# Kernel tuning notes

Hardware: AMD Instinct MI355X
Metric: run time of the kernel (lower is better)

The kernel has to match this reference:

```python
import jax, jax.numpy as jnp
import numpy as np

T = 1024
B = 64
A = 128
ABSTRACT_PENALTY = 0.5
CONSISTENCY_RATIO = 1.0
NEG = -1e30  # acts as log(0) mask; exp underflows to exactly 0 in logsumexp
STOP_IX, CONT_IX = 0, 1


def setup_inputs() -> dict:
    key = jax.random.key(0)
    k1, k2, k3, k4, k5 = jax.random.split(key, 5)
    actions = jax.random.randint(k1, (T,), 0, A, dtype=jnp.int32)
    action_logps = jax.nn.log_softmax(jax.random.normal(k2, (T + 1, B, A), dtype=jnp.float32), axis=-1)
    stop_logps = jax.nn.log_softmax(jax.random.normal(k3, (T + 1, B, 2), dtype=jnp.float32), axis=-1)
    start_logps = jax.nn.log_softmax(jax.random.normal(k4, (T + 1, B), dtype=jnp.float32), axis=-1)
    consistency_penalties = -0.1 * jnp.abs(jax.random.normal(k5, (T + 1, T + 1, B), dtype=jnp.float32))
    return {
        'actions': actions,
        'action_logps': action_logps,
        'stop_logps': stop_logps,
        'start_logps': start_logps,
        'consistency_penalties': consistency_penalties,
    }


def _hsmm_loss(actions, action_logps, stop_logps, start_logps, consistency_penalties):
    T_ = actions.shape[0]
    b = start_logps.shape[1]
    # option_step_dist as fixed (T, b) buffer, rows > current step masked to NEG
    dist0 = jnp.full((T_, b), NEG, dtype=action_logps.dtype).at[0].set(start_logps[0])
    # step i=0: only the action logp (no stop/start rearrange, no consistency pen)
    logp0 = jax.nn.logsumexp(dist0 + action_logps[0, :, actions[0]][None, :])

    idx = jnp.arange(1, T_)
    stop_lps = stop_logps[1:T_, :, STOP_IX]          # (T-1, b)
    cont_lps = stop_logps[1:T_, :, CONT_IX]          # (T-1, b)
    start_lps = start_logps[1:T_]                    # (T-1, b)
    act_lps = action_logps[idx, :, actions[1:]]      # (T-1, b)
    # column i of consistency_penalties, rows :T (masked dist rows kill rows > i)
    cons_cols = jnp.transpose(consistency_penalties[:T_, 1:T_, :], (1, 0, 2))  # (T-1, T, b)

    def step(carry, xs):
        dist, logp, cons = carry
        i, stop_lp, cont_lp, start_lp, act_lp, cp = xs
        total_rearrange = jax.nn.logsumexp(dist + stop_lp[None, :]) - ABSTRACT_PENALTY
        new_mass = start_lp + total_rearrange
        dist = (dist + cont_lp[None, :]).at[i].set(new_mass)
        cons = cons + jax.nn.logsumexp(dist + cp)
        logp = logp + jax.nn.logsumexp(dist + act_lp[None, :])
        return (dist, logp, cons), None

    init = (dist0, logp0, jnp.zeros((), dist0.dtype))
    (dist, logp, cons), _ = jax.lax.scan(step, init, (idx, stop_lps, cont_lps, start_lps, act_lps, cons_cols))
    total_logp = logp + jax.nn.logsumexp(dist + stop_logps[T_, :, STOP_IX][None, :])
    return -total_logp + CONSISTENCY_RATIO * cons


def reference(actions, action_logps, stop_logps, start_logps, consistency_penalties):
    return _hsmm_loss(actions, action_logps, stop_logps, start_logps, consistency_penalties)
```

## Files before the change

kernel.cpp:

```cpp
#include <hip/hip_runtime.h>

#define T_N 1024
#define B_N 64
#define A_N 128
#define TP1 1025

typedef float f32x4 __attribute__((ext_vector_type(4)));

__device__ __forceinline__ float bcf(int x){ return __builtin_bit_cast(float, x); }
__device__ __forceinline__ int   bci(float x){ return __builtin_bit_cast(int, x); }

template<int CTRL, int RM>
__device__ __forceinline__ float dpp_add_step(float x){
  int t = __builtin_amdgcn_update_dpp(0, bci(x), CTRL, RM, 0xf, true);
  return x + bcf(t);
}
__device__ __forceinline__ float wave_sum64(float x){
  x = dpp_add_step<0x111,0xf>(x);
  x = dpp_add_step<0x112,0xf>(x);
  x = dpp_add_step<0x114,0xf>(x);
  x = dpp_add_step<0x118,0xf>(x);
  x = dpp_add_step<0x142,0xa>(x);
  x = dpp_add_step<0x143,0xc>(x);
  return bcf(__builtin_amdgcn_readlane(bci(x), 63));
}
__device__ __forceinline__ void wave_sum64_x2(float a, float b, float& ra, float& rb){
  a = dpp_add_step<0x111,0xf>(a);  b = dpp_add_step<0x111,0xf>(b);
  a = dpp_add_step<0x112,0xf>(a);  b = dpp_add_step<0x112,0xf>(b);
  a = dpp_add_step<0x114,0xf>(a);  b = dpp_add_step<0x114,0xf>(b);
  a = dpp_add_step<0x118,0xf>(a);  b = dpp_add_step<0x118,0xf>(b);
  a = dpp_add_step<0x142,0xa>(a);  b = dpp_add_step<0x142,0xa>(b);
  a = dpp_add_step<0x143,0xc>(a);  b = dpp_add_step<0x143,0xc>(b);
  ra = bcf(__builtin_amdgcn_readlane(bci(a), 63));
  rb = bcf(__builtin_amdgcn_readlane(bci(b), 63));
}
__device__ __forceinline__ float group16_sum(float x){
  x = dpp_add_step<0x111,0xf>(x);
  x = dpp_add_step<0x112,0xf>(x);
  x = dpp_add_step<0x114,0xf>(x);
  x = dpp_add_step<0x118,0xf>(x);
  return x;
}
template<int CTRL, int RM>
__device__ __forceinline__ float dpp_max_step(float x){
  int t = __builtin_amdgcn_update_dpp(bci(-3.4e38f), bci(x), CTRL, RM, 0xf, false);
  return fmaxf(x, bcf(t));
}
__device__ __forceinline__ float wave_max64(float x){
  x = dpp_max_step<0x111,0xf>(x);
  x = dpp_max_step<0x112,0xf>(x);
  x = dpp_max_step<0x114,0xf>(x);
  x = dpp_max_step<0x118,0xf>(x);
  x = dpp_max_step<0x142,0xa>(x);
  x = dpp_max_step<0x143,0xc>(x);
  return bcf(__builtin_amdgcn_readlane(bci(x), 63));
}

__global__ __launch_bounds__(256) void prep_kernel(
    const float* __restrict__ stop_logps,
    const float* __restrict__ start_logps,
    float* __restrict__ pairA,
    float* __restrict__ kap,
    float* __restrict__ cs,
    float* __restrict__ A1p)
{
  const int tid  = (int)threadIdx.x;
  const int lane = tid & 63;
  const int wv   = tid >> 6;
  const int p    = (int)blockIdx.x * 4 + wv;
  const float KAPPA = 0.60653065971263342f;
  const float2* stop2 = (const float2*)stop_logps;

  int g = (int)blockIdx.x * 256 + tid;
  A1p[g] = 0.f;
  A1p[g + 32768] = 0.f;

  if (p < 511) {
    const int i1 = 2 * p + 1, i2 = 2 * p + 2;
    float2 s1 = stop2[i1 * B_N + lane];
    float2 s2 = stop2[i2 * B_N + lane];
    float st1 = start_logps[i1 * B_N + lane];
    float st2 = start_logps[i2 * B_N + lane];
    float esw1 = __expf(s1.x), ecw1 = __expf(s1.y), sv1 = KAPPA * __expf(st1);
    float esw2 = __expf(s2.x), ecw2 = __expf(s2.y), sv2 = KAPPA * __expf(st2);
    float* pb = pairA + (size_t)p * 7 * B_N;
    pb[0 * B_N + lane] = esw1;
    pb[1 * B_N + lane] = ecw1 * esw2;
    pb[2 * B_N + lane] = ecw1 * ecw2;
    pb[3 * B_N + lane] = sv1 * ecw2;
    pb[4 * B_N + lane] = sv1;
    pb[5 * B_N + lane] = sv2;
    pb[6 * B_N + lane] = ecw1;
    float kp = wave_sum64(sv1 * esw2);
    if (lane == 0) kap[p] = kp;
  }

  if (blockIdx.x < 16 && wv == 0) {
    int c = (int)blockIdx.x;
    float s = 0.f;
    for (int k = 1; k <= 64; ++k) {
      int i = 64 * c + k;
      if (i <= 1023) s += stop2[i * B_N + lane].y;
    }
    cs[c * B_N + lane] = s;
  }
}

__global__ __launch_bounds__(64, 1) void scan_kernel(
    const float* __restrict__ stop_logps,
    const float* __restrict__ start_logps,
    const float* __restrict__ pairA,
    const float* __restrict__ kap,
    float* __restrict__ z_ws,
    float* __restrict__ r_ws,
    float* __restrict__ wexp)
{
  const int lane = threadIdx.x;
  float z = __expf(start_logps[lane]);

  float pb[8][7];
  float kp[8];
  #pragma unroll
  for (int q = 0; q < 8; ++q) {
    #pragma unroll
    for (int v = 0; v < 7; ++v) pb[q][v] = pairA[(q * 7 + v) * B_N + lane];
    kp[q] = kap[q];
  }

  for (int P0 = 0; P0 < 504; P0 += 8) {
    #pragma unroll
    for (int q = 0; q < 8; ++q) {
      const int p  = P0 + q;
      const int i1 = 2 * p + 1;
      float A  = pb[q][0], Q  = pb[q][1], CC = pb[q][2], SC = pb[q][3];
      float SV1= pb[q][4], SV2= pb[q][5], E1 = pb[q][6];
      float kpp = kp[q];
      #pragma unroll
      for (int v = 0; v < 7; ++v) pb[q][v] = pairA[((size_t)(p + 8) * 7 + v) * B_N + lane];
      kp[q] = kap[p + 8 < 512 ? p + 8 : 511];

      float d1, d2;
      wave_sum64_x2(z * A, z * Q, d1, d2);
      float r2 = __builtin_fmaf(kpp, d1, d2);
      float z1 = __builtin_fmaf(d1, SV1, z * E1);
      z_ws[i1 * B_N + lane] = z1;
      r_ws[i1]     = d1;
      r_ws[i1 + 1] = r2;
      z = __builtin_fmaf(z, CC, __builtin_fmaf(r2, SV2, d1 * SC));
      z_ws[(i1 + 1) * B_N + lane] = z;

      if (q == 7) {
        int rb  = bci(r2);
        int e16 = ((rb >> 23) & 255) - 127;
        z = ldexpf(z, -e16);
        wexp[p >> 3] = (float)e16;
      }
    }
  }
  #pragma unroll
  for (int q = 0; q < 7; ++q) {
    const int p  = 504 + q;
    const int i1 = 2 * p + 1;
    float A  = pb[q][0], Q  = pb[q][1], CC = pb[q][2], SC = pb[q][3];
    float SV1= pb[q][4], SV2= pb[q][5], E1 = pb[q][6];
    float kpp = kp[q];
    float d1, d2;
    wave_sum64_x2(z * A, z * Q, d1, d2);
    float r2 = __builtin_fmaf(kpp, d1, d2);
    float z1 = __builtin_fmaf(d1, SV1, z * E1);
    z_ws[i1 * B_N + lane] = z1;
    r_ws[i1]     = d1;
    r_ws[i1 + 1] = r2;
    z = __builtin_fmaf(z, CC, __builtin_fmaf(r2, SV2, d1 * SC));
    z_ws[(i1 + 1) * B_N + lane] = z;
  }
  {
    const float KAPPA = 0.60653065971263342f;
    const float2* stop2 = (const float2*)stop_logps;
    float2 sc = stop2[1023 * B_N + lane];
    float  st = start_logps[1023 * B_N + lane];
    float esw = __expf(sc.x), ecw = __expf(sc.y), sv = KAPPA * __expf(st);
    float r = wave_sum64(z * esw);
    z = __builtin_fmaf(sv, r, z * ecw);
    z_ws[1023 * B_N + lane] = z;
    r_ws[1023] = r;
  }
}

__global__ __launch_bounds__(1024) void post_kernel(
    const int* __restrict__ actions,
    const float* __restrict__ action_logps,
    const float* __restrict__ stop_logps,
    const float* __restrict__ start_logps,
    const float* __restrict__ z_ws,
    const float* __restrict__ r_ws,
    const float* __restrict__ wexp,
    const float* __restrict__ cs,
    float* __restrict__ u_ws,
    float* __restrict__ D_ws,
    float* __restrict__ out)
{
  const int tid  = (int)threadIdx.x;
  const int w    = tid >> 6;
  const int lane = tid & 63;
  const float LN2 = 0.69314718055994531f;
  const float2* stop2 = (const float2*)stop_logps;

  __shared__ float Pw[64];
  if (w == 0) {
    float psum = 0.f;
    for (int m = 0; m < lane && m < 63; ++m) psum += wexp[m];
    Pw[lane] = psum * LN2;
  }
  __syncthreads();

  float C = 0.f;
  for (int ww = 0; ww < w; ++ww) C += cs[ww * B_N + lane];
  for (int k = 1; k <= 64; ++k) {
    int i = 64 * w + k;
    if (i > 1023) break;
    C += stop2[i * B_N + lane].y;
    float Pv = Pw[(i - 1) >> 4];
    float R  = __logf(r_ws[i]) + Pv - 0.5f;
    u_ws[i * B_N + lane] = start_logps[i * B_N + lane] + R - C;
    float zs = wave_sum64(z_ws[i * B_N + lane]);
    D_ws[i * B_N + lane] = C - (__logf(zs) + Pv);
  }
  if (tid < 64) u_ws[lane] = start_logps[lane];

  if (w == 15) {
    float st0 = start_logps[lane];
    int   a0  = actions[0];
    float al0 = action_logps[lane * A_N + a0];
    float lp0 = __logf(wave_sum64(__expf(st0 + al0)));
    float stopT = stop_logps[(T_N * B_N + lane) * 2 + 0];
    float z1023 = z_ws[1023 * B_N + lane];
    float fin = __logf(wave_sum64(z1023 * __expf(stopT))) + Pw[63];
    if (lane == 0) out[0] = -(lp0 + fin);
  }
}

__global__ __launch_bounds__(256) void cons_logp_kernel(
    const float* __restrict__ cons_pen,
    const float* __restrict__ u_ws,
    const float* __restrict__ D_ws,
    const int* __restrict__ actions,
    const float* __restrict__ action_logps,
    float* __restrict__ A1p,
    float* __restrict__ LQ)
{
  const int bid  = (int)blockIdx.x;
  const int tid  = (int)threadIdx.x;
  const int lane = tid & 63;
  const int wv   = tid >> 6;

  __shared__ float sm[4][64];
  __shared__ float sa[4][64];

  if (bid < 512) {
    const int bq  = (lane & 15) * 4;
    const int row = lane >> 4;
    #pragma unroll
    for (int t = 0; t < 2; ++t) {
      const int j = t ? (1023 - bid) : bid;
      const float4 u4 = *(const float4*)(u_ws + j * B_N + bq);
      float* dst = A1p + ((j & 63) << 10);
      for (int i0 = j + 4 * wv; i0 <= 1023; i0 += 16) {
        int i  = i0 + row;
        int iL = i > 1023 ? 1023 : i;
        f32x4 cp4 = __builtin_nontemporal_load(
            (const f32x4*)(cons_pen + ((size_t)j * TP1 + iL) * B_N + bq));
        float4 d4  = *(const float4*)(D_ws + (size_t)iL * B_N + bq);
        bool valid = (i >= 1) && (i <= 1023);
        float a0 = u4.x + d4.x + cp4.x;
        float a1 = u4.y + d4.y + cp4.y;
        float a2 = u4.z + d4.z + cp4.z;
        float a3 = u4.w + d4.w + cp4.w;
        a0 = valid ? a0 : -1e30f;
        a1 = valid ? a1 : -1e30f;
        a2 = valid ? a2 : -1e30f;
        a3 = valid ? a3 : -1e30f;
        float sred = (__expf(a0) + __expf(a1)) + (__expf(a2) + __expf(a3));
        sred = group16_sum(sred);
        if (((lane & 15) == 15) && valid) atomicAdd(dst + i, sred);
      }
    }
  } else {
    const int i = 1535 - bid;
    int   ai = actions[i];
    float av = action_logps[((size_t)i * B_N + lane) * A_N + ai];

    float m = -1e30f, acc = 0.f;
    for (int jj = wv; jj <= i; jj += 4) {
      float u  = u_ws[jj * B_N + lane];
      float nm = fmaxf(m, u);
      acc = acc * __expf(m - nm) + __expf(u - nm);
      m = nm;
    }
    sm[wv][lane] = m; sa[wv][lane] = acc;
    __syncthreads();
    if (wv == 0) {
      float m0 = sm[0][lane], m1 = sm[1][lane], m2 = sm[2][lane], m3 = sm[3][lane];
      float M2 = fmaxf(fmaxf(m0, m1), fmaxf(m2, m3));
      float A  = sa[0][lane] * __expf(m0 - M2) + sa[1][lane] * __expf(m1 - M2)
               + sa[2][lane] * __expf(m2 - M2) + sa[3][lane] * __expf(m3 - M2);
      float S  = M2 + __logf(A);
      float val = S + D_ws[(size_t)i * B_N + lane] + av;
      float mx  = wave_max64(val);
      float sum = wave_sum64(__expf(val - mx));
      if (lane == 0) LQ[i] = mx + __logf(sum);
    }
  }
}

__global__ __launch_bounds__(256) void finish_kernel(
    const float* __restrict__ A1p,
    const float* __restrict__ LQ,
    float* __restrict__ out)
{
  const int i = (int)blockIdx.x * 256 + (int)threadIdx.x;
  float v = 0.f;
  if (i >= 1 && i <= 1023) {
    float a = 0.f;
    #pragma unroll 8
    for (int p = 0; p < 64; ++p) a += A1p[(p << 10) + i];
    v = __logf(a) - LQ[i];
  }
  float ws = wave_sum64(v);
  __shared__ float sb[4];
  if ((threadIdx.x & 63) == 0) sb[threadIdx.x >> 6] = ws;
  __syncthreads();
  if (threadIdx.x == 0) atomicAdd(out, sb[0] + sb[1] + sb[2] + sb[3]);
}

extern "C" void kernel_launch(void* const* d_in, const int* in_sizes, int n_in,
                              void* d_out, int out_size, void* d_ws, size_t ws_size,
                              hipStream_t stream) {
  const int*   actions      = (const int*)d_in[0];
  const float* action_logps = (const float*)d_in[1];
  const float* stop_logps   = (const float*)d_in[2];
  const float* start_logps  = (const float*)d_in[3];
  const float* cons_pen     = (const float*)d_in[4];
  float* out = (float*)d_out;

  float* z_ws  = (float*)d_ws;
  float* u_ws  = z_ws + T_N * B_N;
  float* D_ws  = u_ws + T_N * B_N;
  float* A1p   = D_ws + T_N * B_N;
  float* r_ws  = A1p + 64 * 1024;
  float* wexp  = r_ws + T_N;
  float* LQ    = wexp + 64;
  float* cs    = LQ + T_N;
  float* pairA = cs + 16 * B_N;
  float* kap   = pairA + 512 * 7 * B_N;

  hipLaunchKernelGGL(prep_kernel, dim3(128), dim3(256), 0, stream,
                     stop_logps, start_logps, pairA, kap, cs, A1p);
  hipLaunchKernelGGL(scan_kernel, dim3(1), dim3(64), 0, stream,
                     stop_logps, start_logps, pairA, kap, z_ws, r_ws, wexp);
  hipLaunchKernelGGL(post_kernel, dim3(1), dim3(1024), 0, stream,
                     actions, action_logps, stop_logps, start_logps,
                     z_ws, r_ws, wexp, cs, u_ws, D_ws, out);
  hipLaunchKernelGGL(cons_logp_kernel, dim3(1535), dim3(256), 0, stream,
                     cons_pen, u_ws, D_ws, actions, action_logps, A1p, LQ);
  hipLaunchKernelGGL(finish_kernel, dim3(4), dim3(256), 0, stream,
                     A1p, LQ, out);
}
```

Measured before the change: 524.2 us.

## Block the sequential scan four steps at a time with precomputed coupling coefficients

The single-wave sequential scan now advances four time steps per iteration instead of two. Prep precomputes the per-quad products and the cross-step coupling sums, so each iteration needs only one interleaved four-way wave reduction. This shortens the serial dependency chain of DPP reductions on the critical path, at the cost of more prep work and more registers. The r_ws indexing shifts by one and is matched in post_kernel, and the logp accumulation loop in cons_logp_kernel is split into two independent online-logsumexp chains to expose more ILP.

```diff
diff --git a/kernel.cpp b/kernel.cpp
--- a/kernel.cpp
+++ b/kernel.cpp
@@ -24,15 +24,24 @@
   x = dpp_add_step<0x143,0xc>(x);
   return bcf(__builtin_amdgcn_readlane(bci(x), 63));
 }
-__device__ __forceinline__ void wave_sum64_x2(float a, float b, float& ra, float& rb){
-  a = dpp_add_step<0x111,0xf>(a);  b = dpp_add_step<0x111,0xf>(b);
-  a = dpp_add_step<0x112,0xf>(a);  b = dpp_add_step<0x112,0xf>(b);
-  a = dpp_add_step<0x114,0xf>(a);  b = dpp_add_step<0x114,0xf>(b);
-  a = dpp_add_step<0x118,0xf>(a);  b = dpp_add_step<0x118,0xf>(b);
-  a = dpp_add_step<0x142,0xa>(a);  b = dpp_add_step<0x142,0xa>(b);
-  a = dpp_add_step<0x143,0xc>(a);  b = dpp_add_step<0x143,0xc>(b);
+__device__ __forceinline__ void wave_sum64_x4(float a, float b, float c, float d,
+                                              float& ra, float& rb, float& rc, float& rd){
+  a = dpp_add_step<0x111,0xf>(a); b = dpp_add_step<0x111,0xf>(b);
+  c = dpp_add_step<0x111,0xf>(c); d = dpp_add_step<0x111,0xf>(d);
+  a = dpp_add_step<0x112,0xf>(a); b = dpp_add_step<0x112,0xf>(b);
+  c = dpp_add_step<0x112,0xf>(c); d = dpp_add_step<0x112,0xf>(d);
+  a = dpp_add_step<0x114,0xf>(a); b = dpp_add_step<0x114,0xf>(b);
+  c = dpp_add_step<0x114,0xf>(c); d = dpp_add_step<0x114,0xf>(d);
+  a = dpp_add_step<0x118,0xf>(a); b = dpp_add_step<0x118,0xf>(b);
+  c = dpp_add_step<0x118,0xf>(c); d = dpp_add_step<0x118,0xf>(d);
+  a = dpp_add_step<0x142,0xa>(a); b = dpp_add_step<0x142,0xa>(b);
+  c = dpp_add_step<0x142,0xa>(c); d = dpp_add_step<0x142,0xa>(d);
+  a = dpp_add_step<0x143,0xc>(a); b = dpp_add_step<0x143,0xc>(b);
+  c = dpp_add_step<0x143,0xc>(c); d = dpp_add_step<0x143,0xc>(d);
   ra = bcf(__builtin_amdgcn_readlane(bci(a), 63));
   rb = bcf(__builtin_amdgcn_readlane(bci(b), 63));
+  rc = bcf(__builtin_amdgcn_readlane(bci(c), 63));
+  rd = bcf(__builtin_amdgcn_readlane(bci(d), 63));
 }
 __device__ __forceinline__ float group16_sum(float x){
   x = dpp_add_step<0x111,0xf>(x);
@@ -59,8 +68,7 @@
 __global__ __launch_bounds__(256) void prep_kernel(
     const float* __restrict__ stop_logps,
     const float* __restrict__ start_logps,
-    float* __restrict__ pairA,
-    float* __restrict__ kap,
+    float* __restrict__ quadQ,
     float* __restrict__ cs,
     float* __restrict__ A1p)
 {
@@ -72,27 +80,42 @@
   const float2* stop2 = (const float2*)stop_logps;
 
   int g = (int)blockIdx.x * 256 + tid;
-  A1p[g] = 0.f;
-  A1p[g + 32768] = 0.f;
-
-  if (p < 511) {
-    const int i1 = 2 * p + 1, i2 = 2 * p + 2;
-    float2 s1 = stop2[i1 * B_N + lane];
-    float2 s2 = stop2[i2 * B_N + lane];
-    float st1 = start_logps[i1 * B_N + lane];
-    float st2 = start_logps[i2 * B_N + lane];
-    float esw1 = __expf(s1.x), ecw1 = __expf(s1.y), sv1 = KAPPA * __expf(st1);
-    float esw2 = __expf(s2.x), ecw2 = __expf(s2.y), sv2 = KAPPA * __expf(st2);
-    float* pb = pairA + (size_t)p * 7 * B_N;
-    pb[0 * B_N + lane] = esw1;
-    pb[1 * B_N + lane] = ecw1 * esw2;
-    pb[2 * B_N + lane] = ecw1 * ecw2;
-    pb[3 * B_N + lane] = sv1 * ecw2;
-    pb[4 * B_N + lane] = sv1;
-    pb[5 * B_N + lane] = sv2;
-    pb[6 * B_N + lane] = ecw1;
-    float kp = wave_sum64(sv1 * esw2);
-    if (lane == 0) kap[p] = kp;
+  A1p[g] = 0.f; A1p[g + 16384] = 0.f; A1p[g + 32768] = 0.f; A1p[g + 49152] = 0.f;
+
+  if (p < 255) {
+    const int i1 = 4 * p + 1;
+    float2 q1 = stop2[(i1 + 0) * B_N + lane];
+    float2 q2 = stop2[(i1 + 1) * B_N + lane];
+    float2 q3 = stop2[(i1 + 2) * B_N + lane];
+    float2 q4 = stop2[(i1 + 3) * B_N + lane];
+    float t1 = start_logps[(i1 + 0) * B_N + lane];
+    float t2 = start_logps[(i1 + 1) * B_N + lane];
+    float t3 = start_logps[(i1 + 2) * B_N + lane];
+    float t4 = start_logps[(i1 + 3) * B_N + lane];
+    float e1 = __expf(q1.x), c1 = __expf(q1.y), s1 = KAPPA * __expf(t1);
+    float e2 = __expf(q2.x), c2 = __expf(q2.y), s2 = KAPPA * __expf(t2);
+    float e3 = __expf(q3.x), c3 = __expf(q3.y), s3 = KAPPA * __expf(t3);
+    float e4 = __expf(q4.x), c4 = __expf(q4.y), s4 = KAPPA * __expf(t4);
+
+    float V1 = e1;
+    float V2 = e2 * c1;
+    float V3 = e3 * c2 * c1;
+    float V4 = e4 * c3 * c2 * c1;
+
+    float k21 = wave_sum64(e2 * s1);
+    float k31 = wave_sum64(e3 * c2 * s1);
+    float k32 = wave_sum64(e3 * s2);
+    float k41 = wave_sum64(e4 * c3 * c2 * s1);
+    float k42 = wave_sum64(e4 * c3 * s2);
+    float k43 = wave_sum64(e4 * s3);
+
+    f32x4* qs = (f32x4*)quadQ;
+    size_t base = (size_t)p * 5 * 64 + lane;
+    qs[base + 0 * 64] = (f32x4){V1, V2, V3, V4};
+    qs[base + 1 * 64] = (f32x4){c1, s1, c2, s2};
+    qs[base + 2 * 64] = (f32x4){c3, s3, c4, s4};
+    qs[base + 3 * 64] = (f32x4){k21, k31, k32, k41};
+    qs[base + 4 * 64] = (f32x4){k42, k43, 0.f, 0.f};
   }
 
   if (blockIdx.x < 16 && wv == 0) {
@@ -109,81 +132,130 @@
 __global__ __launch_bounds__(64, 1) void scan_kernel(
     const float* __restrict__ stop_logps,
     const float* __restrict__ start_logps,
-    const float* __restrict__ pairA,
-    const float* __restrict__ kap,
+    const float* __restrict__ quadQ,
     float* __restrict__ z_ws,
     float* __restrict__ r_ws,
     float* __restrict__ wexp)
 {
   const int lane = threadIdx.x;
+  const float2* stop2 = (const float2*)stop_logps;
+
+  float2 sct0 = stop2[1021 * B_N + lane];
+  float2 sct1 = stop2[1022 * B_N + lane];
+  float2 sct2 = stop2[1023 * B_N + lane];
+  float stt0 = start_logps[1021 * B_N + lane];
+  float stt1 = start_logps[1022 * B_N + lane];
+  float stt2 = start_logps[1023 * B_N + lane];
+
   float z = __expf(start_logps[lane]);
 
-  float pb[8][7];
-  float kp[8];
+  const f32x4* qs = (const f32x4*)quadQ;
+
+  f32x4 qb[8][5];
   #pragma unroll
-  for (int q = 0; q < 8; ++q) {
+  for (int q = 0; q < 8; ++q)
     #pragma unroll
-    for (int v = 0; v < 7; ++v) pb[q][v] = pairA[(q * 7 + v) * B_N + lane];
-    kp[q] = kap[q];
-  }
-
-  for (int P0 = 0; P0 < 504; P0 += 8) {
+    for (int s = 0; s < 5; ++s)
+      qb[q][s] = qs[((size_t)q * 5 + s) * 64 + lane];
+
+  for (int p0 = 0; p0 < 248; p0 += 8) {
     #pragma unroll
     for (int q = 0; q < 8; ++q) {
-      const int p  = P0 + q;
-      const int i1 = 2 * p + 1;
-      float A  = pb[q][0], Q  = pb[q][1], CC = pb[q][2], SC = pb[q][3];
-      float SV1= pb[q][4], SV2= pb[q][5], E1 = pb[q][6];
-      float kpp = kp[q];
-      #pragma unroll
-      for (int v = 0; v < 7; ++v) pb[q][v] = pairA[((size_t)(p + 8) * 7 + v) * B_N + lane];
-      kp[q] = kap[p + 8 < 512 ? p + 8 : 511];
-
-      float d1, d2;
-      wave_sum64_x2(z * A, z * Q, d1, d2);
-      float r2 = __builtin_fmaf(kpp, d1, d2);
-      float z1 = __builtin_fmaf(d1, SV1, z * E1);
-      z_ws[i1 * B_N + lane] = z1;
-      r_ws[i1]     = d1;
-      r_ws[i1 + 1] = r2;
-      z = __builtin_fmaf(z, CC, __builtin_fmaf(r2, SV2, d1 * SC));
-      z_ws[(i1 + 1) * B_N + lane] = z;
-
-      if (q == 7) {
-        int rb  = bci(r2);
+      const int p  = p0 + q;
+      const int i1 = 4 * p + 1;
+      f32x4 V   = qb[q][0];
+      f32x4 C12 = qb[q][1];
+      f32x4 C34 = qb[q][2];
+      f32x4 K1  = qb[q][3];
+      f32x4 K2  = qb[q][4];
+      {
+        const int pn = p + 8;
+        #pragma unroll
+        for (int s = 0; s < 5; ++s)
+          qb[q][s] = qs[((size_t)pn * 5 + s) * 64 + lane];
+      }
+
+      float d1, d2, d3, d4;
+      wave_sum64_x4(z * V.x, z * V.y, z * V.z, z * V.w, d1, d2, d3, d4);
+      float r1 = d1;
+      float r2 = __builtin_fmaf(K1.x, r1, d2);
+      float r3 = __builtin_fmaf(K1.z, r2, __builtin_fmaf(K1.y, r1, d3));
+      float r4 = __builtin_fmaf(K2.y, r3,
+                 __builtin_fmaf(K2.x, r2, __builtin_fmaf(K1.w, r1, d4)));
+
+      float z1 = __builtin_fmaf(r1, C12.y, z  * C12.x);
+      float z2 = __builtin_fmaf(r2, C12.w, z1 * C12.z);
+      float z3 = __builtin_fmaf(r3, C34.y, z2 * C34.x);
+      float z4 = __builtin_fmaf(r4, C34.w, z3 * C34.z);
+      z_ws[(i1 + 0) * B_N + lane] = z1;
+      z_ws[(i1 + 1) * B_N + lane] = z2;
+      z_ws[(i1 + 2) * B_N + lane] = z3;
+      z_ws[(i1 + 3) * B_N + lane] = z4;
+      if (lane == 0) *(f32x4*)(r_ws + 4 * p) = (f32x4){r1, r2, r3, r4};
+      z = z4;
+
+      if ((q & 3) == 3) {
+        int rb  = bci(r4);
         int e16 = ((rb >> 23) & 255) - 127;
         z = ldexpf(z, -e16);
-        wexp[p >> 3] = (float)e16;
+        if (lane == 0) wexp[p >> 2] = (float)e16;
       }
     }
   }
   #pragma unroll
   for (int q = 0; q < 7; ++q) {
-    const int p  = 504 + q;
-    const int i1 = 2 * p + 1;
-    float A  = pb[q][0], Q  = pb[q][1], CC = pb[q][2], SC = pb[q][3];
-    float SV1= pb[q][4], SV2= pb[q][5], E1 = pb[q][6];
-    float kpp = kp[q];
-    float d1, d2;
-    wave_sum64_x2(z * A, z * Q, d1, d2);
-    float r2 = __builtin_fmaf(kpp, d1, d2);
-    float z1 = __builtin_fmaf(d1, SV1, z * E1);
-    z_ws[i1 * B_N + lane] = z1;
-    r_ws[i1]     = d1;
-    r_ws[i1 + 1] = r2;
-    z = __builtin_fmaf(z, CC, __builtin_fmaf(r2, SV2, d1 * SC));
-    z_ws[(i1 + 1) * B_N + lane] = z;
-  }
+    const int p  = 248 + q;
+    const int i1 = 4 * p + 1;
+    f32x4 V   = qb[q][0];
+    f32x4 C12 = qb[q][1];
+    f32x4 C34 = qb[q][2];
+    f32x4 K1  = qb[q][3];
+    f32x4 K2  = qb[q][4];
+    float d1, d2, d3, d4;
+    wave_sum64_x4(z * V.x, z * V.y, z * V.z, z * V.w, d1, d2, d3, d4);
+    float r1 = d1;
+    float r2 = __builtin_fmaf(K1.x, r1, d2);
+    float r3 = __builtin_fmaf(K1.z, r2, __builtin_fmaf(K1.y, r1, d3));
+    float r4 = __builtin_fmaf(K2.y, r3,
+               __builtin_fmaf(K2.x, r2, __builtin_fmaf(K1.w, r1, d4)));
+    float z1 = __builtin_fmaf(r1, C12.y, z  * C12.x);
+    float z2 = __builtin_fmaf(r2, C12.w, z1 * C12.z);
+    float z3 = __builtin_fmaf(r3, C34.y, z2 * C34.x);
+    float z4 = __builtin_fmaf(r4, C34.w, z3 * C34.z);
+    z_ws[(i1 + 0) * B_N + lane] = z1;
+    z_ws[(i1 + 1) * B_N + lane] = z2;
+    z_ws[(i1 + 2) * B_N + lane] = z3;
+    z_ws[(i1 + 3) * B_N + lane] = z4;
+    if (lane == 0) *(f32x4*)(r_ws + 4 * p) = (f32x4){r1, r2, r3, r4};
+    z = z4;
+    if (q == 3) {
+      int rb  = bci(r4);
+      int e16 = ((rb >> 23) & 255) - 127;
+      z = ldexpf(z, -e16);
+      if (lane == 0) wexp[62] = (float)e16;
+    }
+  }
+  const float KAPPA = 0.60653065971263342f;
   {
-    const float KAPPA = 0.60653065971263342f;
-    const float2* stop2 = (const float2*)stop_logps;
-    float2 sc = stop2[1023 * B_N + lane];
-    float  st = start_logps[1023 * B_N + lane];
-    float esw = __expf(sc.x), ecw = __expf(sc.y), sv = KAPPA * __expf(st);
+    float esw = __expf(sct0.x), ecw = __expf(sct0.y), sv = KAPPA * __expf(stt0);
+    float r = wave_sum64(z * esw);
+    z = __builtin_fmaf(sv, r, z * ecw);
+    z_ws[1021 * B_N + lane] = z;
+    if (lane == 0) r_ws[1020] = r;
+  }
+  {
+    float esw = __expf(sct1.x), ecw = __expf(sct1.y), sv = KAPPA * __expf(stt1);
+    float r = wave_sum64(z * esw);
+    z = __builtin_fmaf(sv, r, z * ecw);
+    z_ws[1022 * B_N + lane] = z;
+    if (lane == 0) r_ws[1021] = r;
+  }
+  {
+    float esw = __expf(sct2.x), ecw = __expf(sct2.y), sv = KAPPA * __expf(stt2);
     float r = wave_sum64(z * esw);
     z = __builtin_fmaf(sv, r, z * ecw);
     z_ws[1023 * B_N + lane] = z;
-    r_ws[1023] = r;
+    if (lane == 0) r_ws[1022] = r;
   }
 }
 
@@ -221,7 +293,7 @@
     if (i > 1023) break;
     C += stop2[i * B_N + lane].y;
     float Pv = Pw[(i - 1) >> 4];
-    float R  = __logf(r_ws[i]) + Pv - 0.5f;
+    float R  = __logf(r_ws[i - 1]) + Pv - 0.5f;
     u_ws[i * B_N + lane] = start_logps[i * B_N + lane] + R - C;
     float zs = wave_sum64(z_ws[i * B_N + lane]);
     D_ws[i * B_N + lane] = C - (__logf(zs) + Pv);
@@ -290,13 +362,21 @@
     int   ai = actions[i];
     float av = action_logps[((size_t)i * B_N + lane) * A_N + ai];
 
-    float m = -1e30f, acc = 0.f;
-    for (int jj = wv; jj <= i; jj += 4) {
-      float u  = u_ws[jj * B_N + lane];
-      float nm = fmaxf(m, u);
-      acc = acc * __expf(m - nm) + __expf(u - nm);
-      m = nm;
-    }
+    float mA = -1e30f, aA = 0.f, mB = -1e30f, aB = 0.f;
+    for (int jj = wv; jj <= i; jj += 8) {
+      float u0 = u_ws[jj * B_N + lane];
+      int   j1 = jj + 4;
+      float u1 = (j1 <= i) ? u_ws[j1 * B_N + lane] : -1e30f;
+      float n0 = fmaxf(mA, u0);
+      aA = aA * __expf(mA - n0) + __expf(u0 - n0);
+      mA = n0;
+      float n1 = fmaxf(mB, u1);
+      aB = aB * __expf(mB - n1) + __expf(u1 - n1);
+      mB = n1;
+    }
+    float m   = fmaxf(mA, mB);
+    float acc = aA * __expf(mA - m) + aB * __expf(mB - m);
+
     sm[wv][lane] = m; sa[wv][lane] = acc;
     __syncthreads();
     if (wv == 0) {
@@ -351,13 +431,12 @@
   float* wexp  = r_ws + T_N;
   float* LQ    = wexp + 64;
   float* cs    = LQ + T_N;
-  float* pairA = cs + 16 * B_N;
-  float* kap   = pairA + 512 * 7 * B_N;
-
-  hipLaunchKernelGGL(prep_kernel, dim3(128), dim3(256), 0, stream,
-                     stop_logps, start_logps, pairA, kap, cs, A1p);
+  float* quadQ = cs + 16 * B_N;
+
+  hipLaunchKernelGGL(prep_kernel, dim3(64), dim3(256), 0, stream,
+                     stop_logps, start_logps, quadQ, cs, A1p);
   hipLaunchKernelGGL(scan_kernel, dim3(1), dim3(64), 0, stream,
-                     stop_logps, start_logps, pairA, kap, z_ws, r_ws, wexp);
+                     stop_logps, start_logps, quadQ, z_ws, r_ws, wexp);
   hipLaunchKernelGGL(post_kernel, dim3(1), dim3(1024), 0, stream,
                      actions, action_logps, stop_logps, start_logps,
                      z_ws, r_ws, wexp, cs, u_ws, D_ws, out);
```

After: 489.7 us. -6.6%, faster.
